# Optimization experiments

Measured on AMD Instinct MI355X. Metric: run time of the kernel, lower is better.

Reference implementation:

```python
import jax, jax.numpy as jnp
import numpy as np


@jax.custom_vjp
def spike(u):
    # Surrogate_BP_Function.forward: u.ge(0).float()
    return (u >= 0).astype(u.dtype)

def _spike_fwd(u):
    return spike(u), u

def _spike_bwd(u, g):
    # backward: g * 0.3 * relu(1 - |u|) * 2
    return (g * 0.6 * jnp.maximum(1.0 - jnp.abs(u), 0.0),)

spike.defvjp(_spike_fwd, _spike_bwd)


def setup_inputs() -> dict:
    key = jax.random.key(0)
    ks = jax.random.split(key, 5)
    B, T, I, H = 64, 512, 256, 512
    x = jax.random.normal(ks[0], (B, T, I), jnp.float32)
    conv1_w = jax.random.normal(ks[1], (H, I, 3), jnp.float32) * 0.1
    conv1_b = jax.random.normal(ks[2], (H,), jnp.float32) * 0.1
    conv2_w = jax.random.normal(ks[3], (H, H, 3), jnp.float32) * 0.1
    conv2_b = jax.random.normal(ks[4], (H,), jnp.float32) * 0.1
    th1 = jnp.ones((), jnp.float32)
    th2 = jnp.ones((), jnp.float32)
    return {"x": x, "conv1_w": conv1_w, "conv1_b": conv1_b,
            "conv2_w": conv2_w, "conv2_b": conv2_b, "th1": th1, "th2": th2}


def reference(x, conv1_w, conv1_b, conv2_w, conv2_b, th1, th2):
    leak = 1.0  # leak_mem from __init__
    # Conv1d(k=3, pad=1) on a length-1 sequence uses only the center tap.
    W1 = conv1_w[:, :, 1]  # [H, I]
    W2 = conv2_w[:, :, 1]  # [H, H]
    B, T, _ = x.shape
    H = W1.shape[0]
    # Precompute input drive for layer 1 (depends only on x[t]).
    z1 = jnp.einsum('bti,hi->bth', x, W1) + conv1_b  # [B, T, H]

    def step(carry, z1_t):
        m1, m2 = carry
        m1 = leak * m1 + z1_t
        thr1 = m1 / th1 - 1.0
        s1 = spike(thr1)
        m1 = m1 - th1 * (thr1 > 0).astype(x.dtype)
        m2 = leak * m2 + s1 @ W2.T + conv2_b
        thr2 = m2 / th2 - 1.0
        s2 = spike(thr2)
        m2 = m2 - th2 * (thr2 > 0).astype(x.dtype)
        return (m1, m2), s2

    init = (jnp.zeros((B, H), x.dtype), jnp.zeros((B, H), x.dtype))
    _, out_t = jax.lax.scan(step, init, jnp.swapaxes(z1, 0, 1))  # [T, B, H]
    return jnp.swapaxes(out_t, 0, 1)  # [B, T, H]
```

## Files before the change

### kernel.cpp

```cpp
#include <hip/hip_runtime.h>

#define BATCH 64
#define TSTEPS 512
#define IDIM 256
#define HDIM 512
#define MROWS (BATCH * TSTEPS)

typedef __attribute__((address_space(1))) const void gvoid;
typedef __attribute__((address_space(3))) void lvoid;

__device__ __forceinline__ void gl2lds16(const void* g, void* l) {
    __builtin_amdgcn_global_load_lds((gvoid*)g, (lvoid*)l, 16, 0, 0);
}

__global__ void extract_weights(const float* __restrict__ c1w,
                                const float* __restrict__ c2w,
                                float* __restrict__ W1T,
                                float* __restrict__ W2T) {
    int tid = blockIdx.x * 256 + threadIdx.x;
    if (tid < IDIM * HDIM) {
        int i = tid >> 9;
        int h = tid & 511;
        W1T[tid] = c1w[(h * IDIM + i) * 3 + 1];
    }
    if (tid < HDIM * HDIM) {
        int h = tid >> 9;
        int j = tid & 511;
        W2T[tid] = c2w[(j * HDIM + h) * 3 + 1];
    }
}

#define BM 128
#define BN 128
#define BK 16

__global__ __launch_bounds__(256, 2) void gemm_f32(const float* __restrict__ A,
                                                   const float* __restrict__ BT,
                                                   const float* __restrict__ bias,
                                                   float* __restrict__ C,
                                                   int K, int addBias) {
    __shared__ __align__(16) float As[BK * BM];
    __shared__ __align__(16) float Bs[BK * BN];

    const int N = HDIM;
    int tid  = threadIdx.x;
    int lane = tid & 63;
    int wave = tid >> 6;
    int row0 = blockIdx.x * BM;
    int col0 = blockIdx.y * BN;
    int wm = (wave >> 1) * 64;
    int wn = (wave & 1) * 64;
    int mbase = wm + (lane >> 3) * 8;
    int nbase = wn + (lane & 7) * 8;

    float acc[8][8];
#pragma unroll
    for (int i = 0; i < 8; i++)
#pragma unroll
        for (int j = 0; j < 8; j++) acc[i][j] = 0.0f;

    int ar = tid >> 1;
    int ak = (tid & 1) * 8;
    const float* ap = A + (size_t)(row0 + ar) * K + ak;

    const char* bp = (const char*)(BT + (size_t)(tid >> 5) * N + col0) + (tid & 31) * 16;
    char* bld = (char*)Bs + tid * 16;
    const size_t bRow8 = (size_t)8 * N * sizeof(float);

    for (int k0 = 0; k0 < K; k0 += BK) {
        gl2lds16(bp, bld);
        gl2lds16(bp + bRow8, bld + 4096);
        float4 a0 = *(const float4*)(ap);
        float4 a1 = *(const float4*)(ap + 4);
        ap += BK;
        bp += (size_t)BK * N * sizeof(float);
        As[(ak + 0) * BM + ar] = a0.x;
        As[(ak + 1) * BM + ar] = a0.y;
        As[(ak + 2) * BM + ar] = a0.z;
        As[(ak + 3) * BM + ar] = a0.w;
        As[(ak + 4) * BM + ar] = a1.x;
        As[(ak + 5) * BM + ar] = a1.y;
        As[(ak + 6) * BM + ar] = a1.z;
        As[(ak + 7) * BM + ar] = a1.w;
        __syncthreads();

#pragma unroll
        for (int k = 0; k < BK; k++) {
            float4 av0 = *(const float4*)&As[k * BM + mbase];
            float4 av1 = *(const float4*)&As[k * BM + mbase + 4];
            float4 bv0 = *(const float4*)&Bs[k * BN + nbase];
            float4 bv1 = *(const float4*)&Bs[k * BN + nbase + 4];
            float a8[8] = {av0.x, av0.y, av0.z, av0.w, av1.x, av1.y, av1.z, av1.w};
            float b8[8] = {bv0.x, bv0.y, bv0.z, bv0.w, bv1.x, bv1.y, bv1.z, bv1.w};
#pragma unroll
            for (int i = 0; i < 8; i++)
#pragma unroll
                for (int j = 0; j < 8; j++)
                    acc[i][j] = fmaf(a8[i], b8[j], acc[i][j]);
        }
        __syncthreads();
    }

    float bb[8];
#pragma unroll
    for (int j = 0; j < 8; j++)
        bb[j] = addBias ? bias[col0 + nbase + j] : 0.0f;
#pragma unroll
    for (int i = 0; i < 8; i++) {
        int row = row0 + mbase + i;
        float4* cp = (float4*)&C[(size_t)row * N + col0 + nbase];
        cp[0] = (float4){acc[i][0] + bb[0], acc[i][1] + bb[1],
                         acc[i][2] + bb[2], acc[i][3] + bb[3]};
        cp[1] = (float4){acc[i][4] + bb[4], acc[i][5] + bb[5],
                         acc[i][6] + bb[6], acc[i][7] + bb[7]};
    }
}

__global__ void lif_scan1(const float* __restrict__ z1,
                          float* __restrict__ s1,
                          const float* __restrict__ th_p) {
    int gtid = blockIdx.x * blockDim.x + threadIdx.x;
    int b = gtid >> 9;
    int h = gtid & 511;
    float th = *th_p;
    const float* zp = z1 + (size_t)b * TSTEPS * HDIM + h;
    float* sp = s1 + (size_t)b * TSTEPS * HDIM + h;
    float m = 0.0f;
    float bufA[16], bufB[16];
#pragma unroll
    for (int i = 0; i < 16; i++) bufA[i] = zp[(size_t)i * HDIM];
    for (int t0 = 0; t0 < TSTEPS; t0 += 32) {
#pragma unroll
        for (int i = 0; i < 16; i++) bufB[i] = zp[(size_t)(t0 + 16 + i) * HDIM];
        {
            float ss[16];
#pragma unroll
            for (int i = 0; i < 16; i++) {
                m += bufA[i];
                float thr = m / th - 1.0f;
                ss[i] = (thr >= 0.0f) ? 1.0f : 0.0f;
                if (thr > 0.0f) m -= th;
            }
#pragma unroll
            for (int i = 0; i < 16; i++) sp[(size_t)(t0 + i) * HDIM] = ss[i];
        }
        if (t0 + 32 < TSTEPS) {
#pragma unroll
            for (int i = 0; i < 16; i++) bufA[i] = zp[(size_t)(t0 + 32 + i) * HDIM];
        }
        {
            float ss[16];
#pragma unroll
            for (int i = 0; i < 16; i++) {
                m += bufB[i];
                float thr = m / th - 1.0f;
                ss[i] = (thr >= 0.0f) ? 1.0f : 0.0f;
                if (thr > 0.0f) m -= th;
            }
#pragma unroll
            for (int i = 0; i < 16; i++) sp[(size_t)(t0 + 16 + i) * HDIM] = ss[i];
        }
    }
}

__global__ void lif_scan2(const float* __restrict__ raw,
                          const float* __restrict__ b2,
                          const float* __restrict__ th_p,
                          float* __restrict__ out) {
    int gtid = blockIdx.x * blockDim.x + threadIdx.x;
    int b = gtid >> 9;
    int j = gtid & 511;
    float th = *th_p;
    float bias = b2[j];
    const float* rp = raw + (size_t)b * TSTEPS * HDIM + j;
    float* op = out + (size_t)b * TSTEPS * HDIM + j;
    float m = 0.0f;
    float bufA[16], bufB[16];
#pragma unroll
    for (int i = 0; i < 16; i++) bufA[i] = rp[(size_t)i * HDIM];
    for (int t0 = 0; t0 < TSTEPS; t0 += 32) {
#pragma unroll
        for (int i = 0; i < 16; i++) bufB[i] = rp[(size_t)(t0 + 16 + i) * HDIM];
        {
            float ss[16];
#pragma unroll
            for (int i = 0; i < 16; i++) {
                m = (m + bufA[i]) + bias;
                float thr = m / th - 1.0f;
                ss[i] = (thr >= 0.0f) ? 1.0f : 0.0f;
                if (thr > 0.0f) m -= th;
            }
#pragma unroll
            for (int i = 0; i < 16; i++) op[(size_t)(t0 + i) * HDIM] = ss[i];
        }
        if (t0 + 32 < TSTEPS) {
#pragma unroll
            for (int i = 0; i < 16; i++) bufA[i] = rp[(size_t)(t0 + 32 + i) * HDIM];
        }
        {
            float ss[16];
#pragma unroll
            for (int i = 0; i < 16; i++) {
                m = (m + bufB[i]) + bias;
                float thr = m / th - 1.0f;
                ss[i] = (thr >= 0.0f) ? 1.0f : 0.0f;
                if (thr > 0.0f) m -= th;
            }
#pragma unroll
            for (int i = 0; i < 16; i++) op[(size_t)(t0 + 16 + i) * HDIM] = ss[i];
        }
    }
}

extern "C" void kernel_launch(void* const* d_in, const int* in_sizes, int n_in,
                              void* d_out, int out_size, void* d_ws, size_t ws_size,
                              hipStream_t stream) {
    const float* x    = (const float*)d_in[0];
    const float* c1w  = (const float*)d_in[1];
    const float* c1b  = (const float*)d_in[2];
    const float* c2w  = (const float*)d_in[3];
    const float* c2b  = (const float*)d_in[4];
    const float* th1  = (const float*)d_in[5];
    const float* th2  = (const float*)d_in[6];
    float* out = (float*)d_out;

    float* W1T  = (float*)d_ws;
    float* W2T  = W1T + IDIM * HDIM;
    float* bufA = W2T + HDIM * HDIM;
    float* bufS = bufA + (size_t)MROWS * HDIM;

    extract_weights<<<(HDIM * HDIM + 255) / 256, 256, 0, stream>>>(c1w, c2w, W1T, W2T);

    {
        dim3 grid(MROWS / BM, HDIM / BN);
        gemm_f32<<<grid, 256, 0, stream>>>(x, W1T, c1b, bufA, IDIM, 1);
    }

    lif_scan1<<<MROWS / 64, 64, 0, stream>>>(bufA, bufS, th1);

    {
        dim3 grid(MROWS / BM, HDIM / BN);
        gemm_f32<<<grid, 256, 0, stream>>>(bufS, W2T, (const float*)nullptr, bufA, HDIM, 0);
    }

    lif_scan2<<<MROWS / 64, 64, 0, stream>>>(bufA, c2b, th2, out);
}
```

Before: 434.7 us.

## Pack layer-1 spikes into bitmasks and replace second GEMM with sparse gather-sum

The first LIF scan now stores its binary spikes as 64-bit ballot masks instead of a dense float matrix. The second dense fp32 GEMM is replaced by a kernel that walks the set bits of each row's mask and sums the matching rows of W2T. This cuts the spike write traffic and skips multiplications by zero or one. The cost depends on spike density and row-gather bandwidth, the ballot adds a store per timestep from lane 0, and the summation order differs from the GEMM, which can change rounding.

```diff
diff --git a/kernel.cpp b/kernel.cpp
--- a/kernel.cpp
+++ b/kernel.cpp
@@ -117,14 +117,16 @@
 }
 
 __global__ void lif_scan1(const float* __restrict__ z1,
-                          float* __restrict__ s1,
+                          unsigned long long* __restrict__ masks,
                           const float* __restrict__ th_p) {
     int gtid = blockIdx.x * blockDim.x + threadIdx.x;
     int b = gtid >> 9;
     int h = gtid & 511;
+    int lane = threadIdx.x & 63;
+    int w = h >> 6;
     float th = *th_p;
     const float* zp = z1 + (size_t)b * TSTEPS * HDIM + h;
-    float* sp = s1 + (size_t)b * TSTEPS * HDIM + h;
+    unsigned long long* mp = masks + (size_t)b * TSTEPS * 8 + w;
     float m = 0.0f;
     float bufA[16], bufB[16];
 #pragma unroll
@@ -133,34 +135,64 @@
 #pragma unroll
         for (int i = 0; i < 16; i++) bufB[i] = zp[(size_t)(t0 + 16 + i) * HDIM];
         {
-            float ss[16];
 #pragma unroll
             for (int i = 0; i < 16; i++) {
                 m += bufA[i];
                 float thr = m / th - 1.0f;
-                ss[i] = (thr >= 0.0f) ? 1.0f : 0.0f;
-                if (thr > 0.0f) m -= th;
-            }
-#pragma unroll
-            for (int i = 0; i < 16; i++) sp[(size_t)(t0 + i) * HDIM] = ss[i];
+                unsigned long long bal = __ballot(thr >= 0.0f);
+                if (lane == 0) mp[(size_t)(t0 + i) * 8] = bal;
+                if (thr > 0.0f) m -= th;
+            }
         }
         if (t0 + 32 < TSTEPS) {
 #pragma unroll
             for (int i = 0; i < 16; i++) bufA[i] = zp[(size_t)(t0 + 32 + i) * HDIM];
         }
         {
-            float ss[16];
 #pragma unroll
             for (int i = 0; i < 16; i++) {
                 m += bufB[i];
                 float thr = m / th - 1.0f;
-                ss[i] = (thr >= 0.0f) ? 1.0f : 0.0f;
-                if (thr > 0.0f) m -= th;
-            }
-#pragma unroll
-            for (int i = 0; i < 16; i++) sp[(size_t)(t0 + 16 + i) * HDIM] = ss[i];
-        }
-    }
+                unsigned long long bal = __ballot(thr >= 0.0f);
+                if (lane == 0) mp[(size_t)(t0 + 16 + i) * 8] = bal;
+                if (thr > 0.0f) m -= th;
+            }
+        }
+    }
+}
+
+__global__ __launch_bounds__(256) void spmm_spikes(
+        const unsigned long long* __restrict__ masks,
+        const float* __restrict__ W2T,
+        float* __restrict__ C) {
+    int lane = threadIdx.x & 63;
+    int wave = threadIdx.x >> 6;
+    int m = blockIdx.x * 4 + wave;
+    const unsigned long long* mrow = masks + (size_t)m * 8;
+
+    float4 s0 = {0.0f, 0.0f, 0.0f, 0.0f};
+    float4 s1 = {0.0f, 0.0f, 0.0f, 0.0f};
+
+    for (int c = 0; c < 8; c++) {
+        unsigned long long mraw = mrow[c];
+        unsigned int lo = __builtin_amdgcn_readfirstlane((unsigned int)mraw);
+        unsigned int hi = __builtin_amdgcn_readfirstlane((unsigned int)(mraw >> 32));
+        unsigned long long mk = ((unsigned long long)hi << 32) | lo;
+        const float* wc = W2T + ((size_t)(c << 6)) * HDIM + lane * 8;
+        while (mk) {
+            int k = __builtin_ctzll(mk);
+            mk &= mk - 1;
+            const float4* wp = (const float4*)(wc + (size_t)k * HDIM);
+            float4 w0 = wp[0];
+            float4 w1 = wp[1];
+            s0.x += w0.x; s0.y += w0.y; s0.z += w0.z; s0.w += w0.w;
+            s1.x += w1.x; s1.y += w1.y; s1.z += w1.z; s1.w += w1.w;
+        }
+    }
+
+    float4* cp = (float4*)(C + (size_t)m * HDIM + lane * 8);
+    cp[0] = s0;
+    cp[1] = s1;
 }
 
 __global__ void lif_scan2(const float* __restrict__ raw,
@@ -227,7 +259,7 @@
     float* W1T  = (float*)d_ws;
     float* W2T  = W1T + IDIM * HDIM;
     float* bufA = W2T + HDIM * HDIM;
-    float* bufS = bufA + (size_t)MROWS * HDIM;
+    unsigned long long* masks = (unsigned long long*)(bufA + (size_t)MROWS * HDIM);
 
     extract_weights<<<(HDIM * HDIM + 255) / 256, 256, 0, stream>>>(c1w, c2w, W1T, W2T);
 
@@ -236,12 +268,9 @@
         gemm_f32<<<grid, 256, 0, stream>>>(x, W1T, c1b, bufA, IDIM, 1);
     }
 
-    lif_scan1<<<MROWS / 64, 64, 0, stream>>>(bufA, bufS, th1);
-
-    {
-        dim3 grid(MROWS / BM, HDIM / BN);
-        gemm_f32<<<grid, 256, 0, stream>>>(bufS, W2T, (const float*)nullptr, bufA, HDIM, 0);
-    }
+    lif_scan1<<<MROWS / 64, 64, 0, stream>>>(bufA, masks, th1);
+
+    spmm_spikes<<<MROWS / 4, 256, 0, stream>>>(masks, W2T, bufA);
 
     lif_scan2<<<MROWS / 64, 64, 0, stream>>>(bufA, c2b, th2, out);
 }
```

Measured after the change: 396.1 us. 8.9% less time.
